# Kernel tuning notes

Hardware: AMD Instinct MI355X
Metric: run time of the kernel (lower is better)

The kernel has to match this reference:

```python
import jax, jax.numpy as jnp
import numpy as np
from jax import lax

GAMMA = 1.0
INF = 1000000.0  # matches the TF code's pseudo-infinity


def _pairwise_sq_dists(a, b):
    # ||a_i - b_j||^2 = ||a||^2 + ||b||^2 - 2 a.b ; avoids the [B,N,M,d] diff tensor
    a2 = jnp.sum(a * a, axis=-1)                      # (B, N)
    b2 = jnp.sum(b * b, axis=-1)                      # (B, M)
    ab = jnp.einsum('bnd,bmd->bnm', a, b)             # (B, N, M)
    return a2[:, :, None] + b2[:, None, :] - 2.0 * ab


def _soft_dtw(seq_a, seq_b, gamma):
    D = _pairwise_sq_dists(seq_a, seq_b)              # (B, N, M)
    B, N, M = D.shape
    dtype = D.dtype
    # row 0 of the DP table: R[0,0]=0, R[0,j>0]=INF
    row0 = jnp.full((B, M + 1), INF, dtype=dtype).at[:, 0].set(0.0)

    def row_step(prev_row, d_i):
        # prev_row: (B, M+1) = R[i-1, :]; d_i: (B, M) = D[:, i-1, :]
        def col_step(left, inputs):
            diag, up, d = inputs                      # each (B,)
            r = jnp.stack([diag, up, left], axis=-1)  # (B, 3)
            softmin = -gamma * jax.nn.logsumexp(-r / gamma, axis=-1)
            val = d + softmin
            return val, val
        left0 = jnp.full((B,), INF, dtype=dtype)      # R[i, 0] = INF
        xs = (prev_row[:, :-1].T, prev_row[:, 1:].T, d_i.T)  # scan over M
        _, vals = lax.scan(col_step, left0, xs)       # (M, B)
        new_row = jnp.concatenate([jnp.full((B, 1), INF, dtype=dtype), vals.T], axis=1)
        return new_row, None

    final_row, _ = lax.scan(row_step, row0, jnp.moveaxis(D, 1, 0))
    return final_row[:, -1]                           # R[N, M]


def setup_inputs() -> dict:
    key = jax.random.key(0)
    k1, k2 = jax.random.split(key)
    B, N, M, d = 128, 384, 384, 128
    seq_a = jax.random.normal(k1, (B, N, d), dtype=jnp.float32)
    seq_b = jax.random.normal(k2, (B, M, d), dtype=jnp.float32)
    return {"seq_a": seq_a, "seq_b": seq_b}


def reference(seq_a, seq_b):
    dist = _soft_dtw(seq_a, seq_b, GAMMA)
    return dist[:, None]                              # (B, 1)
```

## Files before the change

kernel.cpp:

```cpp
#include <hip/hip_runtime.h>
#include <stdint.h>

#define BATCH 128
#define SEQN  384
#define SEQM  384
#define DIM   128
#define KINF   1000000.0f
#define LOG2E  1.4426950408889634f
#define LN2    0.6931471805599453f
#define KINF2  (KINF * LOG2E)
#define NCOLS  388

#define EXP2F(x) __builtin_amdgcn_exp2f(x)
#define LOG2F(x) __builtin_amdgcn_logf(x)

typedef __attribute__((ext_vector_type(8))) short bf16x8;
typedef __attribute__((ext_vector_type(4))) float f32x4;

__device__ __forceinline__ unsigned short bf16_rne(float x) {
    uint32_t u = __float_as_uint(x);
    u += 0x7FFFu + ((u >> 16) & 1u);
    return (unsigned short)(u >> 16);
}
__device__ __forceinline__ uint32_t bf16_pair(float x, float y) {
    uint32_t ux = __float_as_uint(x); ux += 0x7FFFu + ((ux >> 16) & 1u);
    uint32_t uy = __float_as_uint(y); uy += 0x7FFFu + ((uy >> 16) & 1u);
    return (ux >> 16) | (uy & 0xFFFF0000u);
}

__global__ __launch_bounds__(256) void gemm_kernel(
        const float* __restrict__ A, const float* __restrict__ B,
        unsigned short* __restrict__ DtG) {
    __shared__ unsigned short lds[2][128][128];
    __shared__ float normA[128], normB[128];
    const int batch = blockIdx.z;
    const int i0 = blockIdx.x * 128;
    const int j0 = blockIdx.y * 128;
    const int t  = threadIdx.x;

    const float* __restrict__ asrc = A + ((long)batch * SEQN + i0) * DIM;
    const float* __restrict__ bsrc = B + ((long)batch * SEQM + j0) * DIM;

    #pragma unroll
    for (int p = 0; p < 8; p++) {
        int e   = p * 2048 + t * 8;
        int row = e >> 7;
        int grp = (e >> 3) & 15;
        float4 a0 = *(const float4*)(asrc + e);
        float4 a1 = *(const float4*)(asrc + e + 4);
        float4 b0 = *(const float4*)(bsrc + e);
        float4 b1 = *(const float4*)(bsrc + e + 4);
        int sw = (grp ^ (row & 15)) * 8;
        uint4 va, vb;
        va.x = bf16_pair(a0.x, a0.y); va.y = bf16_pair(a0.z, a0.w);
        va.z = bf16_pair(a1.x, a1.y); va.w = bf16_pair(a1.z, a1.w);
        vb.x = bf16_pair(b0.x, b0.y); vb.y = bf16_pair(b0.z, b0.w);
        vb.z = bf16_pair(b1.x, b1.y); vb.w = bf16_pair(b1.z, b1.w);
        *(uint4*)&lds[0][row][sw] = va;
        *(uint4*)&lds[1][row][sw] = vb;
        float sa = a0.x*a0.x + a0.y*a0.y + a0.z*a0.z + a0.w*a0.w
                 + a1.x*a1.x + a1.y*a1.y + a1.z*a1.z + a1.w*a1.w;
        float sb = b0.x*b0.x + b0.y*b0.y + b0.z*b0.z + b0.w*b0.w
                 + b1.x*b1.x + b1.y*b1.y + b1.z*b1.z + b1.w*b1.w;
        #pragma unroll
        for (int off = 8; off > 0; off >>= 1) {
            sa += __shfl_down(sa, off, 16);
            sb += __shfl_down(sb, off, 16);
        }
        if ((t & 15) == 0) { normA[row] = sa; normB[row] = sb; }
    }
    __syncthreads();

    const int wave = t >> 6, lane = t & 63;
    const int iq = (wave & 1) * 64;
    const int jq = (wave >> 1) * 64;
    const int l16 = lane & 15, q = lane >> 4;

    f32x4 acc[4][4] = {};
    #pragma unroll
    for (int kk = 0; kk < 4; kk++) {
        bf16x8 af[4], bfr[4];
        #pragma unroll
        for (int s = 0; s < 4; s++) {
            int arow = iq + s * 16 + l16;
            af[s]  = *(const bf16x8*)&lds[0][arow][((kk * 4 + q) ^ (arow & 15)) * 8];
            int brow = jq + s * 16 + l16;
            bfr[s] = *(const bf16x8*)&lds[1][brow][((kk * 4 + q) ^ (brow & 15)) * 8];
        }
        #pragma unroll
        for (int si = 0; si < 4; si++)
            #pragma unroll
            for (int sj = 0; sj < 4; sj++)
                acc[si][sj] = __builtin_amdgcn_mfma_f32_16x16x32_bf16(
                                  af[si], bfr[sj], acc[si][sj], 0, 0, 0);
    }

    unsigned short* __restrict__ Dt = DtG + (long)batch * NCOLS * SEQN;
    #pragma unroll
    for (int sj = 0; sj < 4; sj++) {
        int j = j0 + jq + sj * 16 + l16;
        float bn = normB[jq + sj * 16 + l16];
        unsigned short* drow = Dt + (long)j * SEQN;
        #pragma unroll
        for (int si = 0; si < 4; si++) {
            int i = i0 + iq + si * 16 + q * 4;
            float4 an = *(const float4*)&normA[iq + si * 16 + q * 4];
            ushort4 pack;
            pack.x = bf16_rne((an.x + bn - 2.0f * acc[si][sj][0]) * LOG2E);
            pack.y = bf16_rne((an.y + bn - 2.0f * acc[si][sj][1]) * LOG2E);
            pack.z = bf16_rne((an.z + bn - 2.0f * acc[si][sj][2]) * LOG2E);
            pack.w = bf16_rne((an.w + bn - 2.0f * acc[si][sj][3]) * LOG2E);
            *(ushort4*)(drow + i) = pack;
        }
    }

    if (blockIdx.y == 0) {
        uint32_t pv = bf16_pair(KINF2, KINF2);
        int c = 384 + (t >> 6);
        int i = i0 + ((t & 63) << 1);
        *(uint32_t*)(Dt + (long)c * SEQN + i) = pv;
    }
}

__global__ __launch_bounds__(64) void dtw_kernel(
        const unsigned short* __restrict__ Dt, float* __restrict__ out) {
    const int b = blockIdx.x;
    const int t = threadIdx.x;
    const unsigned short* __restrict__ dtb =
        Dt + (long)b * NCOLS * SEQN + 6 * t;

    float prev[6];
    #pragma unroll
    for (int r = 0; r < 6; r++) prev[r] = KINF2;

    uint3 dslot[4];
    #pragma unroll
    for (int q = 0; q < 4; q++) {
        int c = q - 2 * t;
        int cc = c < 0 ? 0 : c;
        dslot[q] = *(const uint3*)(dtb + (long)cc * SEQN);
    }

    float rcv0 = KINF2, rcv1 = KINF2, old_diag = KINF2;
    float lane0_diag = 0.0f;
    const bool isl0 = (t == 0);
    int c0 = -2 * t;

#define UNPACK(d, w)                                                        \
    d[0] = __uint_as_float(w.x << 16);                                      \
    d[1] = __uint_as_float(w.x & 0xFFFF0000u);                              \
    d[2] = __uint_as_float(w.y << 16);                                      \
    d[3] = __uint_as_float(w.y & 0xFFFF0000u);                              \
    d[4] = __uint_as_float(w.z << 16);                                      \
    d[5] = __uint_as_float(w.z & 0xFFFF0000u);

#define COLPASS(dX, diag0, upseed, LEFTV, NEWV)                             \
    {                                                                       \
        float Bp = (upseed), Fp = 1.0f;                                     \
        float Bv[6], Fv[6];                                                 \
        _Pragma("unroll")                                                   \
        for (int r = 0; r < 6; r++) {                                       \
            float vd = (r == 0) ? (diag0) : LEFTV[r - 1];                   \
            float vl = LEFTV[r];                                            \
            float m3 = fminf(fminf(vd, vl), Bp);            \
            float al = EXP2F(m3 - Bp);                                      \
            float be = EXP2F(m3 - vd) + EXP2F(m3 - vl);                     \
            float Fr = __builtin_fmaf(al, Fp, be);                          \
            float Br = dX[r] + m3;                                          \
            Bv[r] = Br; Fv[r] = Fr;                                         \
            Bp = Br; Fp = Fr;                                               \
        }                                                                   \
        _Pragma("unroll")                                                   \
        for (int r = 0; r < 6; r++)                                         \
            NEWV[r] = Bv[r] - LOG2F(Fv[r]);                                 \
    }

#define PHASE2(Q)                                                           \
    {                                                                       \
        uint3 wA = dslot[Q];                                                \
        uint3 wB = dslot[(Q) + 1];                                          \
        {               \
            int cnA = c0 + 4;                                               \
            int ccA = cnA < 0 ? 0 : (cnA > 387 ? 387 : cnA);                \
            int cnB = c0 + 5;                                               \
            int ccB = cnB < 0 ? 0 : (cnB > 387 ? 387 : cnB);                \
            dslot[Q]       = *(const uint3*)(dtb + (long)ccA * SEQN);       \
            dslot[(Q) + 1] = *(const uint3*)(dtb + (long)ccB * SEQN);       \
        }                                                                   \
        float dA[6], dB[6];                                                 \
        UNPACK(dA, wA)                                                      \
        UNPACK(dB, wB)                                                      \
        float dgA = isl0 ? lane0_diag : old_diag;                           \
        float upA = isl0 ? KINF2 : rcv0;                                    \
        float upB = isl0 ? KINF2 : rcv1;                                    \
        float newA[6];                                                      \
        COLPASS(dA, dgA, upA, prev, newA)                                   \
        COLPASS(dB, upA, upB, newA, prev)                                   \
        old_diag = rcv1;                                                    \
        rcv0 = __shfl_up(newA[5], 1, 64);                                   \
        rcv1 = __shfl_up(prev[5], 1, 64);                                   \
        lane0_diag = KINF2;                                                 \
        c0 += 2;                                                            \
    }

    for (int pp = 0; pp < 127; pp++) {
        PHASE2(0)
        PHASE2(2)
    }
    PHASE2(0)
#undef PHASE2
#undef COLPASS
#undef UNPACK

    if (t == 63) out[b] = prev[5] * LN2;
}

extern "C" void kernel_launch(void* const* d_in, const int* in_sizes, int n_in,
                              void* d_out, int out_size, void* d_ws, size_t ws_size,
                              hipStream_t stream) {
    (void)in_sizes; (void)n_in; (void)out_size; (void)ws_size;
    const float* a = (const float*)d_in[0];
    const float* b = (const float*)d_in[1];
    float* out = (float*)d_out;

    unsigned short* Dmat = (unsigned short*)d_ws;

    gemm_kernel<<<dim3(SEQN / 128, SEQM / 128, BATCH), dim3(256), 0, stream>>>(
        a, b, Dmat);
    dtw_kernel<<<dim3(BATCH), dim3(64), 0, stream>>>(Dmat, out);
}
```

Before: 217.3 us.

## Fuse distance GEMM and soft-DTW into one producer-consumer kernel with LDS ring

Merges the GEMM and DTW kernels into a single per-batch workgroup. Three producer waves compute 32-column chunks of the distance matrix with MFMA directly into an LDS ring buffer, while one consumer wave runs the wavefront DP, synchronised through workgroup-scope atomic flags. This removes the global-memory round trip for the bf16 distance matrix and the second launch, and overlaps GEMM work with the serial DP. The costs are spin-wait polling with a timeout-break, producers reading A from global memory redundantly for every chunk, and only 128 workgroups on the device.

```diff
diff --git a/kernel.cpp b/kernel.cpp
--- a/kernel.cpp
+++ b/kernel.cpp
@@ -9,7 +9,10 @@
 #define LOG2E  1.4426950408889634f
 #define LN2    0.6931471805599453f
 #define KINF2  (KINF * LOG2E)
-#define NCOLS  388
+
+#define RING    204
+#define RSTRIDE 392
+#define NCHUNK  13
 
 #define EXP2F(x) __builtin_amdgcn_exp2f(x)
 #define LOG2F(x) __builtin_amdgcn_logf(x)
@@ -28,106 +31,134 @@
     return (ux >> 16) | (uy & 0xFFFF0000u);
 }
 
-__global__ __launch_bounds__(256) void gemm_kernel(
+union frag_u { bf16x8 v; uint32_t u[4]; };
+
+__global__ __launch_bounds__(256) void fused_dtw(
         const float* __restrict__ A, const float* __restrict__ B,
-        unsigned short* __restrict__ DtG) {
-    __shared__ unsigned short lds[2][128][128];
-    __shared__ float normA[128], normB[128];
-    const int batch = blockIdx.z;
-    const int i0 = blockIdx.x * 128;
-    const int j0 = blockIdx.y * 128;
-    const int t  = threadIdx.x;
-
-    const float* __restrict__ asrc = A + ((long)batch * SEQN + i0) * DIM;
-    const float* __restrict__ bsrc = B + ((long)batch * SEQM + j0) * DIM;
-
-    #pragma unroll
-    for (int p = 0; p < 8; p++) {
-        int e   = p * 2048 + t * 8;
-        int row = e >> 7;
-        int grp = (e >> 3) & 15;
-        float4 a0 = *(const float4*)(asrc + e);
-        float4 a1 = *(const float4*)(asrc + e + 4);
-        float4 b0 = *(const float4*)(bsrc + e);
-        float4 b1 = *(const float4*)(bsrc + e + 4);
-        int sw = (grp ^ (row & 15)) * 8;
-        uint4 va, vb;
-        va.x = bf16_pair(a0.x, a0.y); va.y = bf16_pair(a0.z, a0.w);
-        va.z = bf16_pair(a1.x, a1.y); va.w = bf16_pair(a1.z, a1.w);
-        vb.x = bf16_pair(b0.x, b0.y); vb.y = bf16_pair(b0.z, b0.w);
-        vb.z = bf16_pair(b1.x, b1.y); vb.w = bf16_pair(b1.z, b1.w);
-        *(uint4*)&lds[0][row][sw] = va;
-        *(uint4*)&lds[1][row][sw] = vb;
-        float sa = a0.x*a0.x + a0.y*a0.y + a0.z*a0.z + a0.w*a0.w
-                 + a1.x*a1.x + a1.y*a1.y + a1.z*a1.z + a1.w*a1.w;
-        float sb = b0.x*b0.x + b0.y*b0.y + b0.z*b0.z + b0.w*b0.w
-                 + b1.x*b1.x + b1.y*b1.y + b1.z*b1.z + b1.w*b1.w;
-        #pragma unroll
-        for (int off = 8; off > 0; off >>= 1) {
-            sa += __shfl_down(sa, off, 16);
-            sb += __shfl_down(sb, off, 16);
+        float* __restrict__ out) {
+    __shared__ __align__(16) unsigned short ring[RING * RSTRIDE];
+    __shared__ __align__(16) float normA[SEQN];
+    __shared__ int prod_done[16];
+    __shared__ int cons_pp;
+
+    const int bat  = blockIdx.x;
+    const int tid  = threadIdx.x;
+    const int wv   = tid >> 6;
+    const int lane = tid & 63;
+
+    if (tid < 16) prod_done[tid] = 0;
+    if (tid == 16) cons_pp = -1;
+    __syncthreads();
+
+    if (wv != 0) {
+        const int l16 = lane & 15, q = lane >> 4;
+        const float* __restrict__ Ab = A + (long)bat * SEQN * DIM;
+        const float* __restrict__ Bb = B + (long)bat * SEQM * DIM;
+        bool first = true;
+        for (int k = wv - 1; k < NCHUNK; k += 3) {
+            if (k >= 6) {
+                int thr = 8 * k - 9, g = 0;
+                while (__hip_atomic_load(&cons_pp, __ATOMIC_ACQUIRE,
+                                         __HIP_MEMORY_SCOPE_WORKGROUP) < thr)
+                    if (++g > (1 << 22)) break;
+            }
+            if (k == 12) {
+                uint32_t pv = bf16_pair(KINF2, KINF2);
+                #pragma unroll
+                for (int c = 0; c < 4; c++) {
+                    uint32_t* p = (uint32_t*)&ring[(384 - RING + c) * RSTRIDE + 6 * lane];
+                    p[0] = pv; p[1] = pv; p[2] = pv;
+                }
+            } else {
+                frag_u bfrag[2][4];
+                float bn[2];
+                #pragma unroll
+                for (int jg = 0; jg < 2; jg++) {
+                    const float* bp = Bb + (long)(32 * k + jg * 16 + l16) * DIM + q * 8;
+                    float s = 0.0f;
+                    #pragma unroll
+                    for (int kk = 0; kk < 4; kk++) {
+                        float4 v0 = *(const float4*)(bp + kk * 32);
+                        float4 v1 = *(const float4*)(bp + kk * 32 + 4);
+                        bfrag[jg][kk].u[0] = bf16_pair(v0.x, v0.y);
+                        bfrag[jg][kk].u[1] = bf16_pair(v0.z, v0.w);
+                        bfrag[jg][kk].u[2] = bf16_pair(v1.x, v1.y);
+                        bfrag[jg][kk].u[3] = bf16_pair(v1.z, v1.w);
+                        s += v0.x*v0.x + v0.y*v0.y + v0.z*v0.z + v0.w*v0.w
+                           + v1.x*v1.x + v1.y*v1.y + v1.z*v1.z + v1.w*v1.w;
+                    }
+                    s += __shfl_xor(s, 16, 64);
+                    s += __shfl_xor(s, 32, 64);
+                    bn[jg] = s;
+                }
+                for (int si = 0; si < 24; si++) {
+                    const float* ap = Ab + (long)(si * 16 + l16) * DIM + q * 8;
+                    float4 a0[4], a1[4];
+                    #pragma unroll
+                    for (int kk = 0; kk < 4; kk++) {
+                        a0[kk] = *(const float4*)(ap + kk * 32);
+                        a1[kk] = *(const float4*)(ap + kk * 32 + 4);
+                    }
+                    frag_u afr[4];
+                    #pragma unroll
+                    for (int kk = 0; kk < 4; kk++) {
+                        afr[kk].u[0] = bf16_pair(a0[kk].x, a0[kk].y);
+                        afr[kk].u[1] = bf16_pair(a0[kk].z, a0[kk].w);
+                        afr[kk].u[2] = bf16_pair(a1[kk].x, a1[kk].y);
+                        afr[kk].u[3] = bf16_pair(a1[kk].z, a1[kk].w);
+                    }
+                    if (first) {
+                        float sa = 0.0f;
+                        #pragma unroll
+                        for (int kk = 0; kk < 4; kk++)
+                            sa += a0[kk].x*a0[kk].x + a0[kk].y*a0[kk].y
+                                + a0[kk].z*a0[kk].z + a0[kk].w*a0[kk].w
+                                + a1[kk].x*a1[kk].x + a1[kk].y*a1[kk].y
+                                + a1[kk].z*a1[kk].z + a1[kk].w*a1[kk].w;
+                        sa += __shfl_xor(sa, 16, 64);
+                        sa += __shfl_xor(sa, 32, 64);
+                        if (q == 0) normA[si * 16 + l16] = sa;
+                    }
+                    f32x4 acc0 = {0.0f, 0.0f, 0.0f, 0.0f};
+                    f32x4 acc1 = {0.0f, 0.0f, 0.0f, 0.0f};
+                    #pragma unroll
+                    for (int kk = 0; kk < 4; kk++) {
+                        acc0 = __builtin_amdgcn_mfma_f32_16x16x32_bf16(
+                                   afr[kk].v, bfrag[0][kk].v, acc0, 0, 0, 0);
+                        acc1 = __builtin_amdgcn_mfma_f32_16x16x32_bf16(
+                                   afr[kk].v, bfrag[1][kk].v, acc1, 0, 0, 0);
+                    }
+                    if (first) asm volatile("s_waitcnt lgkmcnt(0)" ::: "memory");
+                    float4 an = *(const float4*)&normA[si * 16 + q * 4];
+                    #pragma unroll
+                    for (int jg = 0; jg < 2; jg++) {
+                        int col  = 32 * k + jg * 16 + l16;
+                        int slot = col >= RING ? col - RING : col;
+                        f32x4 ac = jg ? acc1 : acc0;
+                        ushort4 pk;
+                        pk.x = bf16_rne((an.x + bn[jg] - 2.0f * ac[0]) * LOG2E);
+                        pk.y = bf16_rne((an.y + bn[jg] - 2.0f * ac[1]) * LOG2E);
+                        pk.z = bf16_rne((an.z + bn[jg] - 2.0f * ac[2]) * LOG2E);
+                        pk.w = bf16_rne((an.w + bn[jg] - 2.0f * ac[3]) * LOG2E);
+                        *(ushort4*)&ring[slot * RSTRIDE + si * 16 + q * 4] = pk;
+                    }
+                }
+                first = false;
+            }
+            __hip_atomic_store(&prod_done[k], 1, __ATOMIC_RELEASE,
+                               __HIP_MEMORY_SCOPE_WORKGROUP);
         }
-        if ((t & 15) == 0) { normA[row] = sa; normB[row] = sb; }
-    }
-    __syncthreads();
-
-    const int wave = t >> 6, lane = t & 63;
-    const int iq = (wave & 1) * 64;
-    const int jq = (wave >> 1) * 64;
-    const int l16 = lane & 15, q = lane >> 4;
-
-    f32x4 acc[4][4] = {};
-    #pragma unroll
-    for (int kk = 0; kk < 4; kk++) {
-        bf16x8 af[4], bfr[4];
-        #pragma unroll
-        for (int s = 0; s < 4; s++) {
-            int arow = iq + s * 16 + l16;
-            af[s]  = *(const bf16x8*)&lds[0][arow][((kk * 4 + q) ^ (arow & 15)) * 8];
-            int brow = jq + s * 16 + l16;
-            bfr[s] = *(const bf16x8*)&lds[1][brow][((kk * 4 + q) ^ (brow & 15)) * 8];
-        }
-        #pragma unroll
-        for (int si = 0; si < 4; si++)
-            #pragma unroll
-            for (int sj = 0; sj < 4; sj++)
-                acc[si][sj] = __builtin_amdgcn_mfma_f32_16x16x32_bf16(
-                                  af[si], bfr[sj], acc[si][sj], 0, 0, 0);
-    }
-
-    unsigned short* __restrict__ Dt = DtG + (long)batch * NCOLS * SEQN;
-    #pragma unroll
-    for (int sj = 0; sj < 4; sj++) {
-        int j = j0 + jq + sj * 16 + l16;
-        float bn = normB[jq + sj * 16 + l16];
-        unsigned short* drow = Dt + (long)j * SEQN;
-        #pragma unroll
-        for (int si = 0; si < 4; si++) {
-            int i = i0 + iq + si * 16 + q * 4;
-            float4 an = *(const float4*)&normA[iq + si * 16 + q * 4];
-            ushort4 pack;
-            pack.x = bf16_rne((an.x + bn - 2.0f * acc[si][sj][0]) * LOG2E);
-            pack.y = bf16_rne((an.y + bn - 2.0f * acc[si][sj][1]) * LOG2E);
-            pack.z = bf16_rne((an.z + bn - 2.0f * acc[si][sj][2]) * LOG2E);
-            pack.w = bf16_rne((an.w + bn - 2.0f * acc[si][sj][3]) * LOG2E);
-            *(ushort4*)(drow + i) = pack;
-        }
-    }
-
-    if (blockIdx.y == 0) {
-        uint32_t pv = bf16_pair(KINF2, KINF2);
-        int c = 384 + (t >> 6);
-        int i = i0 + ((t & 63) << 1);
-        *(uint32_t*)(Dt + (long)c * SEQN + i) = pv;
-    }
-}
-
-__global__ __launch_bounds__(64) void dtw_kernel(
-        const unsigned short* __restrict__ Dt, float* __restrict__ out) {
-    const int b = blockIdx.x;
-    const int t = threadIdx.x;
-    const unsigned short* __restrict__ dtb =
-        Dt + (long)b * NCOLS * SEQN + 6 * t;
+        return;
+    }
+
+    const int t = lane;
+    {
+        int g = 0;
+        while (__hip_atomic_load(&prod_done[0], __ATOMIC_ACQUIRE,
+                                 __HIP_MEMORY_SCOPE_WORKGROUP) == 0)
+            if (++g > (1 << 22)) break;
+    }
+    const unsigned short* __restrict__ ringT = ring + 6 * t;
 
     float prev[6];
     #pragma unroll
@@ -135,10 +166,10 @@
 
     uint3 dslot[4];
     #pragma unroll
-    for (int q = 0; q < 4; q++) {
-        int c = q - 2 * t;
+    for (int qq = 0; qq < 4; qq++) {
+        int c = qq - 2 * t;
         int cc = c < 0 ? 0 : c;
-        dslot[q] = *(const uint3*)(dtb + (long)cc * SEQN);
+        dslot[qq] = *(const uint3*)(ringT + cc * RSTRIDE);
     }
 
     float rcv0 = KINF2, rcv1 = KINF2, old_diag = KINF2;
@@ -179,13 +210,15 @@
     {                                                                       \
         uint3 wA = dslot[Q];                                                \
         uint3 wB = dslot[(Q) + 1];                                          \
-        {               \
+        {            \
             int cnA = c0 + 4;                                               \
             int ccA = cnA < 0 ? 0 : (cnA > 387 ? 387 : cnA);                \
+            int sA  = ccA >= RING ? ccA - RING : ccA;                       \
             int cnB = c0 + 5;                                               \
             int ccB = cnB < 0 ? 0 : (cnB > 387 ? 387 : cnB);                \
-            dslot[Q]       = *(const uint3*)(dtb + (long)ccA * SEQN);       \
-            dslot[(Q) + 1] = *(const uint3*)(dtb + (long)ccB * SEQN);       \
+            int sB  = ccB >= RING ? ccB - RING : ccB;                       \
+            dslot[Q]       = *(const uint3*)(ringT + sA * RSTRIDE);         \
+            dslot[(Q) + 1] = *(const uint3*)(ringT + sB * RSTRIDE);         \
         }                                                                   \
         float dA[6], dB[6];                                                 \
         UNPACK(dA, wA)                                                      \
@@ -204,28 +237,36 @@
     }
 
     for (int pp = 0; pp < 127; pp++) {
+        if ((pp & 7) == 7) {
+            int k = (4 * pp + 7) >> 5;
+            if (k < NCHUNK) {
+                int g = 0;
+                while (__hip_atomic_load(&prod_done[k], __ATOMIC_ACQUIRE,
+                                         __HIP_MEMORY_SCOPE_WORKGROUP) == 0)
+                    if (++g > (1 << 22)) break;
+            }
+        }
         PHASE2(0)
         PHASE2(2)
+        if (t == 0)
+            __hip_atomic_store(&cons_pp, pp,
+                               __ATOMIC_RELEASE, __HIP_MEMORY_SCOPE_WORKGROUP);
     }
     PHASE2(0)
 #undef PHASE2
 #undef COLPASS
 #undef UNPACK
 
-    if (t == 63) out[b] = prev[5] * LN2;
+    if (t == 63) out[bat] = prev[5] * LN2;
 }
 
 extern "C" void kernel_launch(void* const* d_in, const int* in_sizes, int n_in,
                               void* d_out, int out_size, void* d_ws, size_t ws_size,
                               hipStream_t stream) {
-    (void)in_sizes; (void)n_in; (void)out_size; (void)ws_size;
+    (void)in_sizes; (void)n_in; (void)out_size; (void)d_ws; (void)ws_size;
     const float* a = (const float*)d_in[0];
     const float* b = (const float*)d_in[1];
     float* out = (float*)d_out;
 
-    unsigned short* Dmat = (unsigned short*)d_ws;
-
-    gemm_kernel<<<dim3(SEQN / 128, SEQM / 128, BATCH), dim3(256), 0, stream>>>(
-        a, b, Dmat);
-    dtw_kernel<<<dim3(BATCH), dim3(64), 0, stream>>>(Dmat, out);
-}
+    fused_dtw<<<dim3(BATCH), dim3(256), 0, stream>>>(a, b, out);
+}
```

After: 276.0 us. 27.0% more time.
